# Kernel optimization log

Hardware: AMD Instinct MI355X
Metric: run time of the kernel (lower is better)

The kernel has to match this reference:

```python
import jax, jax.numpy as jnp
import numpy as np

N_NODES = 100000
N_EDGES = 1600000
K_IND = 16          # num_indicator_weight (distance bins)
K_MLP = 16          # num_mlp_weight
DIM_HIDDEN = 64     # dim_mlp_hidden
DIST_MAX = 1.0      # distance_max
K = K_IND + K_MLP   # node feature dim / Dense output dim


def setup_inputs() -> dict:
    key = jax.random.key(0)
    ks = jax.random.split(key, 10)
    nodes = jax.random.normal(ks[0], (N_NODES, K), dtype=jnp.float32)
    distance = jax.random.uniform(ks[1], (N_EDGES,), dtype=jnp.float32) * DIST_MAX
    receivers = jnp.sort(jax.random.randint(ks[2], (N_EDGES,), 0, N_NODES, dtype=jnp.int32))
    senders = jax.random.randint(ks[3], (N_EDGES,), 0, N_NODES, dtype=jnp.int32)
    edges_padding = jnp.ones((N_EDGES,), dtype=jnp.float32)
    # MLPWeights params (Dense(1->H), Dense(H->K_MLP))
    w1 = jax.random.normal(ks[4], (1, DIM_HIDDEN), dtype=jnp.float32) / np.sqrt(1.0)
    b1 = jnp.zeros((DIM_HIDDEN,), dtype=jnp.float32)
    w2 = jax.random.normal(ks[5], (DIM_HIDDEN, K_MLP), dtype=jnp.float32) / np.sqrt(DIM_HIDDEN)
    b2 = jnp.zeros((K_MLP,), dtype=jnp.float32)
    # PowerDifference params (a=0.5, b=2)
    a = jnp.array([0.5], dtype=jnp.float32)
    b = jnp.array([2.0], dtype=jnp.float32)
    # gamma_self (no bias), gamma_gathered (with bias), both Dense(K->K)
    wg_self = jax.random.normal(ks[6], (K, K), dtype=jnp.float32) / np.sqrt(K)
    wg_gath = jax.random.normal(ks[7], (K, K), dtype=jnp.float32) / np.sqrt(K)
    bg_gath = jnp.zeros((K,), dtype=jnp.float32)
    return {"nodes": nodes, "distance": distance, "edges_padding": edges_padding,
            "receivers": receivers, "senders": senders,
            "w1": w1, "b1": b1, "w2": w2, "b2": b2,
            "a": a, "b": b, "wg_self": wg_self, "wg_gath": wg_gath, "bg_gath": bg_gath}


def _normalize_edges(edges, seg_ids, num_segments):
    sums = jax.ops.segment_sum(edges, seg_ids, num_segments=num_segments, indices_are_sorted=True)
    return edges / (sums[seg_ids] + 1e-5)


def _softmax_edges(edges, seg_ids, num_segments):
    maxs = jax.ops.segment_max(edges, seg_ids, num_segments=num_segments, indices_are_sorted=True)
    e = jnp.exp(edges - maxs[seg_ids])
    sums = jax.ops.segment_sum(e, seg_ids, num_segments=num_segments, indices_are_sorted=True)
    return e / sums[seg_ids]


def reference(nodes, distance, edges_padding, receivers, senders,
              w1, b1, w2, b2, a, b, wg_self, wg_gath, bg_gath):
    n = nodes.shape[0]
    d = distance[:, None]                                   # [E,1]
    # IndicatorWeights: bin membership via heaviside of product
    bins = jnp.linspace(0.0, DIST_MAX, K_IND + 1, dtype=nodes.dtype)
    indicator = jnp.heaviside((bins[None, :-1] - d) * (d - bins[None, 1:]), 0.0)  # [E,K_IND]
    indicator_w = _normalize_edges(indicator, receivers, n)
    # MLPWeights: Dense -> relu -> Dense, then segment softmax
    mlp = jax.nn.relu(d @ w1 + b1) @ w2 + b2                # [E,K_MLP]
    mlp_w = _softmax_edges(mlp, receivers, n)
    weights = jnp.concatenate([indicator_w, mlp_w], axis=1) * edges_padding[:, None]  # [E,K]
    # PowerDifference on gathered node pairs
    a_c = jnp.clip(a, 0.0, 1.0)
    b_c = jnp.abs(b)
    edge_pds = jnp.power(jnp.abs(a_c * nodes[receivers] - (1.0 - a_c) * nodes[senders]), b_c)  # [E,K]
    gathered = jax.ops.segment_sum(weights * edge_pds, receivers, num_segments=n, indices_are_sorted=True)  # [N,K]
    out = jax.nn.relu(nodes @ wg_self + (gathered @ wg_gath + bg_gath))
    return out
```

## Files before the change

kernel.cpp:

```cpp
#include <hip/hip_runtime.h>
#include <math.h>

#define K_TOT 32
#define K_IND 16
#define K_MLP 16
#define DHID  64
#define M_NODES 4
#define LOG2E 1.44269504088896340736f

template<bool B> struct BoolC { static constexpr bool value = B; };

__device__ __forceinline__ float fast_rcp(float x) {
    float r; asm("v_rcp_f32 %0, %1" : "=v"(r) : "v"(x)); return r;
}
__device__ __forceinline__ float fast_exp2(float x) {
    float r; asm("v_exp_f32 %0, %1" : "=v"(r) : "v"(x)); return r;
}


__global__ void prep_kernel(const int* __restrict__ recv, int E, int N,
                            const float* __restrict__ w1,
                            const float* __restrict__ b1,
                            const float* __restrict__ w2,
                            const float* __restrict__ padv,
                            float* __restrict__ wsP,
                            float* __restrict__ wsN,
                            int* __restrict__ wsflag,
                            int* __restrict__ viol,
                            int* __restrict__ rp) {
    if (blockIdx.x == 0 && threadIdx.x < 64) {
        int t = threadIdx.x;
        if (t < K_MLP) {
            float P = 0.f, Nn = 0.f;
            for (int j = 0; j < DHID; ++j) {
                float w = w1[j];
                float v = w2[j * K_MLP + t];
                P  += fmaxf(w, 0.f) * v;
                Nn += fminf(w, 0.f) * v;
            }
            wsP[t] = P; wsN[t] = Nn;
        }
        bool nz = (b1[t] != 0.f);
        unsigned long long mask = __ballot(nz);
        if (t == 0) *wsflag = (mask == 0ull) ? 1 : 0;
    }
    int e = blockIdx.x * blockDim.x + threadIdx.x;
    bool ok = (e < E) ? (padv[e] == 1.0f) : true;
    if (!__all((int)ok)) {
        if ((threadIdx.x & 63) == 0) atomicOr(viol, 1);
    }
    if (e < E) {
        int r0 = recv[e];
        int r1 = (e + 1 < E) ? recv[e + 1] : N;
        if (e == 0) {
            for (int t = 0; t <= r0; ++t) rp[t] = 0;
        }
        for (int t = r0 + 1; t <= r1; ++t) rp[t] = e + 1;
    }
}

__global__ __launch_bounds__(256) void graph_kernel(
        const float* __restrict__ nodes,
        const float* __restrict__ dist,
        const float* __restrict__ padv,
        const int*   __restrict__ send,
        const float* __restrict__ w1,
        const float* __restrict__ b1,
        const float* __restrict__ w2,
        const float* __restrict__ b2,
        const float* __restrict__ a_p,
        const float* __restrict__ b_p,
        const float* __restrict__ wg_self,
        const float* __restrict__ wg_gath,
        const float* __restrict__ bg,
        const float* __restrict__ wsP,
        const float* __restrict__ wsN,
        const int*   __restrict__ wsflag,
        const int*   __restrict__ viol,
        const int*   __restrict__ rp,
        float* __restrict__ out,
        int N, int E) {
    __shared__ __align__(16) float2 s_wp[1024];
    __shared__ __align__(16) float2 s_gn[4][32][4];

    {
        int t = threadIdx.x;
        float4 ws4 = ((const float4*)wg_self)[t];
        float4 wg4 = ((const float4*)wg_gath)[t];
        s_wp[t * 4 + 0] = make_float2(ws4.x, wg4.x);
        s_wp[t * 4 + 1] = make_float2(ws4.y, wg4.y);
        s_wp[t * 4 + 2] = make_float2(ws4.z, wg4.z);
        s_wp[t * 4 + 3] = make_float2(ws4.w, wg4.w);
    }
    __syncthreads();

    int wv   = threadIdx.x >> 6;
    int wave = blockIdx.x * 4 + wv;
    int n0   = wave * M_NODES;
    if (n0 >= N) return;

    int lane = threadIdx.x & 63;
    int eg   = lane >> 4;
    int cc   = lane & 15;

    float a_c = fminf(fmaxf(a_p[0], 0.f), 1.f);
    float am  = 1.f - a_c;
    float bc  = fabsf(b_p[0]);

    float Pk = wsP[cc];
    float Nk = wsN[cc];
    float Pk2 = Pk * LOG2E;
    float Nk2 = Nk * LOG2E;
    float negM2 = -fmaxf(fabsf(Pk2), fabsf(Nk2));

    float lo = (float)cc * 0.0625f;
    float hi = lo + 0.0625f;

    int fastflag = (*wsflag != 0) && (bc == 2.0f);
    int allpad   = (*viol == 0);
    float bgv = bg[lane & 31];

    int rl = rp[min(n0 + min(lane, 4), N)];
    int e0k[5];
#pragma unroll
    for (int k = 0; k < 5; ++k) e0k[k] = __shfl(rl, k);
    int lenk[4]; int maxlen = 0;
#pragma unroll
    for (int k = 0; k < 4; ++k) {
        lenk[k] = e0k[k + 1] - e0k[k];
        maxlen = max(maxlen, lenk[k]);
    }

    int cap = N * K_TOT - 1;
    float rowA = nodes[min(n0 * K_TOT + lane, cap)];
    float rowB = nodes[min(n0 * K_TOT + 64 + lane, cap)];

    auto fast4 = [&](auto APC) {
        constexpr bool ALLPAD = decltype(APC)::value;
        float dC, peC = 1.f; int sC;
        {
            int li = min(lane, max(lenk[0] - 1, 0));
            int ei = min(e0k[0] + li, E - 1);
            dC = dist[ei]; sC = send[ei];
            if (!ALLPAD) peC = padv[ei];
        }
#pragma unroll
        for (int k = 0; k < 4; ++k) {
            float dNx = 0.f, peNx = 1.f; int sNx = 0;
            if (k < 3) {
                int li = min(lane, max(lenk[k + 1] - 1, 0));
                int ei = min(e0k[k + 1] + li, E - 1);
                dNx = dist[ei]; sNx = send[ei];
                if (!ALLPAD) peNx = padv[ei];
            }
            int len = lenk[k];
            float d_all  = (lane < len) ? dC : 2.0f;
            int   s_all  = sC;
            float pe_all = peC;
            (void)pe_all;

            float nsrc = (k < 2) ? rowA : rowB;
            float nr0 = __shfl(nsrc, (k & 1) * 32 + cc);
            float nr1 = __shfl(nsrc, (k & 1) * 32 + cc + 16);
            float anr0 = a_c * nr0;
            float anr1 = a_c * nr1;

            float cnt = 0.f, si = 0.f, l = 0.f, acc = 0.f;
            if (len > 0) {
                int nG = (len + 3) >> 2;

#define GRP_BODY(G)                                                          \
                {                                                            \
                    int i = ((G) << 2) + eg;                                 \
                    bool valid = i < len;                                    \
                    float d  = __shfl(d_all, i);                             \
                    int   s  = __shfl(s_all, i);                             \
                    float pe = ALLPAD ? 1.0f : __shfl(pe_all, i);            \
                    const float* nsrow = nodes + (s * K_TOT + cc);           \
                    float ns0 = nsrow[0];                                    \
                    float ns1 = nsrow[16];                                   \
                    float t0 = fmaf(-am, ns0, anr0);                         \
                    float t1 = fmaf(-am, ns1, anr1);                         \
                    float pd0 = t0 * t0;                                     \
                    float pd1 = t1 * t1;                                     \
                    bool inb = (d > lo) && (d < hi);                         \
                    if (ALLPAD) {                                            \
                        float mb = inb ? 1.f : 0.f;                          \
                        cnt += mb;                                           \
                        si   = fmaf(mb, pd0, si);                            \
                    } else {                                                 \
                        cnt += inb ? 1.f : 0.f;                              \
                        si   = inb ? fmaf(pe, pd0, si) : si;                 \
                    }                                                        \
                    float q2 = (d > 0.f) ? Pk2 : Nk2;                        \
                    float p = fast_exp2(fmaf(d, q2, negM2));                 \
                    p = valid ? p : 0.f;                                     \
                    l += p;                                                  \
                    acc = ALLPAD ? fmaf(p, pd1, acc)                         \
                                 : fmaf(p, pe * pd1, acc);                   \
                }

                int g = 0;
                for (; g + 2 <= nG; g += 2) {
                    GRP_BODY(g)
                    GRP_BODY(g + 1)
                }
                if (g < nG) {
                    GRP_BODY(g)
                }
#undef GRP_BODY
            }

#pragma unroll
            for (int off = 16; off <= 32; off <<= 1) {
                cnt += __shfl_xor(cnt, off);
                si  += __shfl_xor(si,  off);
                l   += __shfl_xor(l,   off);
                acc += __shfl_xor(acc, off);
            }
            float g_ind = si * fast_rcp(cnt + 1e-5f);
            float g_mlp = (l > 0.f) ? (acc * fast_rcp(l)) : 0.f;

            float pre_g = ((lane >> 4) & 1) ? g_mlp : g_ind;
            float pre_n = ((lane >> 4) & 1) ? nr1 : nr0;
            if (lane < 32) s_gn[wv][lane][k] = make_float2(pre_n, pre_g);

            dC = dNx; sC = sNx; peC = peNx;
        }
    };

    if (__builtin_amdgcn_readfirstlane((int)(fastflag && (maxlen <= 64)))) {
        if (__builtin_amdgcn_readfirstlane(allpad)) fast4(BoolC<true>{});
        else                                        fast4(BoolC<false>{});
    } else {
        for (int k = 0; k < 4; ++k) {
            int len = lenk[k], e0 = e0k[k];
            float nsrc = (k < 2) ? rowA : rowB;
            float nr0 = __shfl(nsrc, (k & 1) * 32 + cc);
            float nr1 = __shfl(nsrc, (k & 1) * 32 + cc + 16);
            float anr0 = a_c * nr0;
            float anr1 = a_c * nr1;

            float cnt = 0.f, si = 0.f, l = 0.f, acc = 0.f;
            float m_on = -INFINITY;
            for (int i = eg; i < len; i += 4) {
                int e = e0 + i;
                float d  = dist[e];
                int   s  = send[e];
                float pe = padv[e];
                const float* nsrow = nodes + (s * K_TOT + cc);
                float ns0 = nsrow[0];
                float ns1 = nsrow[16];
                float t0 = fabsf(fmaf(-am, ns0, anr0));
                float t1 = fabsf(fmaf(-am, ns1, anr1));
                float pd0 = powf(t0, bc);
                float pd1 = powf(t1, bc);

                bool inb = (d > lo) && (d < hi);
                cnt += inb ? 1.f : 0.f;
                si  += inb ? pe * pd0 : 0.f;

                float mlp = 0.f;
                for (int j = 0; j < DHID; ++j) {
                    float h2 = fmaxf(fmaf(d, w1[j], b1[j]), 0.f);
                    mlp = fmaf(h2, w2[j * K_MLP + cc], mlp);
                }
                float mn = fmaxf(m_on, mlp);
                float al = (m_on == -INFINITY) ? 0.f : __expf(m_on - mn);
                float p  = __expf(mlp - mn);
                l   = fmaf(l, al, p);
                acc = fmaf(acc, al, p * pe * pd1);
                m_on = mn;
            }
#pragma unroll
            for (int off = 16; off <= 32; off <<= 1) {
                cnt += __shfl_xor(cnt, off);
                si  += __shfl_xor(si,  off);
                float m2 = __shfl_xor(m_on, off), l2 = __shfl_xor(l, off), a2 = __shfl_xor(acc, off);
                float mn = fmaxf(m_on, m2);
                float f1 = (m_on == -INFINITY) ? 0.f : __expf(m_on - mn);
                float f2 = (m2   == -INFINITY) ? 0.f : __expf(m2 - mn);
                l   = l * f1 + l2 * f2;
                acc = acc * f1 + a2 * f2;
                m_on = mn;
            }
            float g_ind = si / (cnt + 1e-5f);
            float g_mlp = (l > 0.f) ? (acc / l) : 0.f;

            float pre_g = ((lane >> 4) & 1) ? g_mlp : g_ind;
            float pre_n = ((lane >> 4) & 1) ? nr1 : nr0;
            if (lane < 32) s_gn[wv][lane][k] = make_float2(pre_n, pre_g);
        }
    }

    int h  = lane >> 5;
    int oc = lane & 31;
    const float2* wpp = &s_wp[(h * 16) * K_TOT + oc];
    const float2 (* __restrict__ sgw)[4] = s_gn[wv];

    float o0 = 0.f, o1 = 0.f, o2 = 0.f, o3 = 0.f;
#pragma unroll
    for (int jj = 0; jj < 16; ++jj) {
        float2 w   = wpp[jj * K_TOT];
        float4 v01 = *reinterpret_cast<const float4*>(&sgw[h * 16 + jj][0]);
        float4 v23 = *reinterpret_cast<const float4*>(&sgw[h * 16 + jj][2]);
        o0 = fmaf(v01.x, w.x, o0); o0 = fmaf(v01.y, w.y, o0);
        o1 = fmaf(v01.z, w.x, o1); o1 = fmaf(v01.w, w.y, o1);
        o2 = fmaf(v23.x, w.x, o2); o2 = fmaf(v23.y, w.y, o2);
        o3 = fmaf(v23.z, w.x, o3); o3 = fmaf(v23.w, w.y, o3);
    }
    o0 += __shfl_xor(o0, 32);
    o1 += __shfl_xor(o1, 32);
    o2 += __shfl_xor(o2, 32);
    o3 += __shfl_xor(o3, 32);
    o0 = fmaxf(o0 + bgv, 0.f);
    o1 = fmaxf(o1 + bgv, 0.f);
    o2 = fmaxf(o2 + bgv, 0.f);
    o3 = fmaxf(o3 + bgv, 0.f);

    float st0 = (lane >= 32) ? o1 : o0;
    float st1 = (lane >= 32) ? o3 : o2;
    int   b5  = lane >> 5;
    if (n0 + b5 < N)     out[n0 * K_TOT + lane]      = st0;
    if (n0 + 2 + b5 < N) out[n0 * K_TOT + 64 + lane] = st1;
}

extern "C" void kernel_launch(void* const* d_in, const int* in_sizes, int n_in,
                              void* d_out, int out_size, void* d_ws, size_t ws_size,
                              hipStream_t stream) {
    const float* nodes   = (const float*)d_in[0];
    const float* dist    = (const float*)d_in[1];
    const float* padv    = (const float*)d_in[2];
    const int*   recv    = (const int*)d_in[3];
    const int*   send    = (const int*)d_in[4];
    const float* w1      = (const float*)d_in[5];
    const float* b1      = (const float*)d_in[6];
    const float* w2      = (const float*)d_in[7];
    const float* b2      = (const float*)d_in[8];
    const float* a_p     = (const float*)d_in[9];
    const float* b_p     = (const float*)d_in[10];
    const float* wg_self = (const float*)d_in[11];
    const float* wg_gath = (const float*)d_in[12];
    const float* bg      = (const float*)d_in[13];
    float* out = (float*)d_out;

    int N = in_sizes[0] / K_TOT;
    int E = in_sizes[1];

    float* wsf    = (float*)d_ws;
    float* wsP    = wsf;
    float* wsN    = wsf + 16;
    int*   wsflag = (int*)d_ws + 32;
    int*   viol   = (int*)d_ws + 33;
    int*   rp     = (int*)d_ws + 64;

    hipMemsetAsync(viol, 0, sizeof(int), stream);

    prep_kernel<<<(E + 255) / 256, 256, 0, stream>>>(recv, E, N, w1, b1, w2,
                                                     padv, wsP, wsN, wsflag,
                                                     viol, rp);
    int waves = (N + M_NODES - 1) / M_NODES;
    graph_kernel<<<(waves + 3) / 4, 256, 0, stream>>>(
        nodes, dist, padv, send, w1, b1, w2, b2, a_p, b_p,
        wg_self, wg_gath, bg, wsP, wsN, wsflag, viol, rp, out, N, E);
}
```

Baseline: 144.5 us.

## Load edge data directly per group and specialize softmax for nonnegative distances

The fast path no longer stages distance and sender values in registers and broadcasts them with shuffles. Each edge group now loads dist/send straight from memory at a wave-uniform base, and a touch-prefetch warms the next node's edges. The prep kernel also checks that all distances are nonnegative, which lets the simple path drop the sign select and use a tighter softmax shift. The maxlen<=64 limit goes away, and node rows are loaded with scalar-uniform addresses instead of shuffles. This trades shuffle traffic for more direct global loads and adds one extra pass over dist in prep.

```diff
diff --git a/kernel.cpp b/kernel.cpp
--- a/kernel.cpp
+++ b/kernel.cpp
@@ -23,6 +23,7 @@
                             const float* __restrict__ b1,
                             const float* __restrict__ w2,
                             const float* __restrict__ padv,
+                            const float* __restrict__ dist,
                             float* __restrict__ wsP,
                             float* __restrict__ wsN,
                             int* __restrict__ wsflag,
@@ -45,9 +46,13 @@
         if (t == 0) *wsflag = (mask == 0ull) ? 1 : 0;
     }
     int e = blockIdx.x * blockDim.x + threadIdx.x;
-    bool ok = (e < E) ? (padv[e] == 1.0f) : true;
-    if (!__all((int)ok)) {
+    bool okp = (e < E) ? (padv[e] == 1.0f) : true;
+    if (!__all((int)okp)) {
         if ((threadIdx.x & 63) == 0) atomicOr(viol, 1);
+    }
+    bool okd = (e < E) ? (dist[e] >= 0.0f) : true;
+    if (!__all((int)okd)) {
+        if ((threadIdx.x & 63) == 0) atomicOr(viol, 2);
     }
     if (e < E) {
         int r0 = recv[e];
@@ -111,104 +116,128 @@
     float Nk = wsN[cc];
     float Pk2 = Pk * LOG2E;
     float Nk2 = Nk * LOG2E;
-    float negM2 = -fmaxf(fabsf(Pk2), fabsf(Nk2));
+    float negMs = -fabsf(Pk2);
+    float negMg = fminf(negMs, -fabsf(Nk2));
 
     float lo = (float)cc * 0.0625f;
     float hi = lo + 0.0625f;
 
     int fastflag = (*wsflag != 0) && (bc == 2.0f);
-    int allpad   = (*viol == 0);
+    int simple   = fastflag && (*viol == 0);
     float bgv = bg[lane & 31];
 
     int rl = rp[min(n0 + min(lane, 4), N)];
     int e0k[5];
 #pragma unroll
     for (int k = 0; k < 5; ++k) e0k[k] = __shfl(rl, k);
-    int lenk[4]; int maxlen = 0;
-#pragma unroll
-    for (int k = 0; k < 4; ++k) {
-        lenk[k] = e0k[k + 1] - e0k[k];
-        maxlen = max(maxlen, lenk[k]);
-    }
-
-    int cap = N * K_TOT - 1;
-    float rowA = nodes[min(n0 * K_TOT + lane, cap)];
-    float rowB = nodes[min(n0 * K_TOT + 64 + lane, cap)];
-
-    auto fast4 = [&](auto APC) {
-        constexpr bool ALLPAD = decltype(APC)::value;
-        float dC, peC = 1.f; int sC;
-        {
-            int li = min(lane, max(lenk[0] - 1, 0));
-            int ei = min(e0k[0] + li, E - 1);
-            dC = dist[ei]; sC = send[ei];
-            if (!ALLPAD) peC = padv[ei];
-        }
+    int lenk[4];
+#pragma unroll
+    for (int k = 0; k < 4; ++k) lenk[k] = e0k[k + 1] - e0k[k];
+
+    auto fast4 = [&](auto SC) {
+        constexpr bool SIMPLE = decltype(SC)::value;
+        int nu0 = __builtin_amdgcn_readfirstlane(min(n0, N - 1));
+        float nr0C = nodes[nu0 * K_TOT + cc];
+        float nr1C = nodes[nu0 * K_TOT + cc + 16];
 #pragma unroll
         for (int k = 0; k < 4; ++k) {
-            float dNx = 0.f, peNx = 1.f; int sNx = 0;
+            float nr0N = 0.f, nr1N = 0.f;
             if (k < 3) {
-                int li = min(lane, max(lenk[k + 1] - 1, 0));
-                int ei = min(e0k[k + 1] + li, E - 1);
-                dNx = dist[ei]; sNx = send[ei];
-                if (!ALLPAD) peNx = padv[ei];
+                int nu1 = __builtin_amdgcn_readfirstlane(min(n0 + k + 1, N - 1));
+                nr0N = nodes[nu1 * K_TOT + cc];
+                nr1N = nodes[nu1 * K_TOT + cc + 16];
+                int pfi = min(e0k[k + 1] + (lane & 48), E - 1);
+                float dpf = dist[pfi];
+                int   spf = send[pfi];
+                asm volatile("" :: "v"(dpf), "v"(spf));
             }
             int len = lenk[k];
-            float d_all  = (lane < len) ? dC : 2.0f;
-            int   s_all  = sC;
-            float pe_all = peC;
-            (void)pe_all;
-
-            float nsrc = (k < 2) ? rowA : rowB;
-            float nr0 = __shfl(nsrc, (k & 1) * 32 + cc);
-            float nr1 = __shfl(nsrc, (k & 1) * 32 + cc + 16);
-            float anr0 = a_c * nr0;
-            float anr1 = a_c * nr1;
+            int e0u = __builtin_amdgcn_readfirstlane(e0k[k]);
+            const float* db = dist + e0u;
+            const int*   sb = send + e0u;
+            const float* pb = padv + e0u;
+            (void)pb;
+
+            float anr0 = a_c * nr0C;
+            float anr1 = a_c * nr1C;
 
             float cnt = 0.f, si = 0.f, l = 0.f, acc = 0.f;
-            if (len > 0) {
-                int nG = (len + 3) >> 2;
-
-#define GRP_BODY(G)                                                          \
-                {                                                            \
-                    int i = ((G) << 2) + eg;                                 \
-                    bool valid = i < len;                                    \
-                    float d  = __shfl(d_all, i);                             \
-                    int   s  = __shfl(s_all, i);                             \
-                    float pe = ALLPAD ? 1.0f : __shfl(pe_all, i);            \
-                    const float* nsrow = nodes + (s * K_TOT + cc);           \
-                    float ns0 = nsrow[0];                                    \
-                    float ns1 = nsrow[16];                                   \
-                    float t0 = fmaf(-am, ns0, anr0);                         \
-                    float t1 = fmaf(-am, ns1, anr1);                         \
-                    float pd0 = t0 * t0;                                     \
-                    float pd1 = t1 * t1;                                     \
-                    bool inb = (d > lo) && (d < hi);                         \
-                    if (ALLPAD) {                                            \
-                        float mb = inb ? 1.f : 0.f;                          \
-                        cnt += mb;                                           \
-                        si   = fmaf(mb, pd0, si);                            \
-                    } else {                                                 \
-                        cnt += inb ? 1.f : 0.f;                              \
-                        si   = inb ? fmaf(pe, pd0, si) : si;                 \
-                    }                                                        \
+
+#define FB(G)                                                                \
+            {                                                                \
+                int idx = ((G) << 2) + eg;                                   \
+                float d  = db[idx];                                          \
+                int   s  = sb[idx];                                          \
+                float pe = SIMPLE ? 1.0f : pb[idx];                          \
+                const float* nsrow = nodes + (s * K_TOT + cc);               \
+                float ns0 = nsrow[0];                                        \
+                float ns1 = nsrow[16];                                       \
+                float t0 = fmaf(-am, ns0, anr0);                             \
+                float t1 = fmaf(-am, ns1, anr1);                             \
+                float pd0 = t0 * t0;                                         \
+                float pd1 = t1 * t1;                                         \
+                bool inb = (d > lo) && (d < hi);                             \
+                if (SIMPLE) {                                                \
+                    float mb = inb ? 1.f : 0.f;                              \
+                    cnt += mb;                                               \
+                    si   = fmaf(mb, pd0, si);                                \
+                    float p = fast_exp2(fmaf(d, Pk2, negMs));                \
+                    l += p;                                                  \
+                    acc = fmaf(p, pd1, acc);                                 \
+                } else {                                                     \
+                    cnt += inb ? 1.f : 0.f;                                  \
+                    si   = inb ? fmaf(pe, pd0, si) : si;                     \
                     float q2 = (d > 0.f) ? Pk2 : Nk2;                        \
-                    float p = fast_exp2(fmaf(d, q2, negM2));                 \
-                    p = valid ? p : 0.f;                                     \
+                    float p = fast_exp2(fmaf(d, q2, negMg));                 \
                     l += p;                                                  \
-                    acc = ALLPAD ? fmaf(p, pd1, acc)                         \
-                                 : fmaf(p, pe * pd1, acc);                   \
+                    acc = fmaf(p, pe * pd1, acc);                            \
+                }                                                            \
+            }
+
+            int nGf = len >> 2;
+            int rem = len & 3;
+            int g = 0;
+            for (; g + 2 <= nGf; g += 2) {
+                FB(g)
+                FB(g + 1)
+            }
+            if (g < nGf) {
+                FB(g)
+            }
+#undef FB
+            if (rem) {
+                int i  = (nGf << 2) + eg;
+                int ii = min(i, len - 1);
+                float d  = db[ii];
+                int   s  = sb[ii];
+                float pe = SIMPLE ? 1.0f : pb[ii];
+                const float* nsrow = nodes + (s * K_TOT + cc);
+                float ns0 = nsrow[0];
+                float ns1 = nsrow[16];
+                float t0 = fmaf(-am, ns0, anr0);
+                float t1 = fmaf(-am, ns1, anr1);
+                float pd0 = t0 * t0;
+                float pd1 = t1 * t1;
+                bool valid = i < len;
+                bool inb = valid && (d > lo) && (d < hi);
+                float p;
+                if (SIMPLE) {
+                    float mb = inb ? 1.f : 0.f;
+                    cnt += mb;
+                    si   = fmaf(mb, pd0, si);
+                    p = fast_exp2(fmaf(d, Pk2, negMs));
+                    p = valid ? p : 0.f;
+                    l += p;
+                    acc = fmaf(p, pd1, acc);
+                } else {
+                    cnt += inb ? 1.f : 0.f;
+                    si   = inb ? fmaf(pe, pd0, si) : si;
+                    float q2 = (d > 0.f) ? Pk2 : Nk2;
+                    p = fast_exp2(fmaf(d, q2, negMg));
+                    p = valid ? p : 0.f;
+                    l += p;
+                    acc = fmaf(p, pe * pd1, acc);
                 }
-
-                int g = 0;
-                for (; g + 2 <= nG; g += 2) {
-                    GRP_BODY(g)
-                    GRP_BODY(g + 1)
-                }
-                if (g < nG) {
-                    GRP_BODY(g)
-                }
-#undef GRP_BODY
             }
 
 #pragma unroll
@@ -222,22 +251,22 @@
             float g_mlp = (l > 0.f) ? (acc * fast_rcp(l)) : 0.f;
 
             float pre_g = ((lane >> 4) & 1) ? g_mlp : g_ind;
-            float pre_n = ((lane >> 4) & 1) ? nr1 : nr0;
+            float pre_n = ((lane >> 4) & 1) ? nr1C : nr0C;
             if (lane < 32) s_gn[wv][lane][k] = make_float2(pre_n, pre_g);
 
-            dC = dNx; sC = sNx; peC = peNx;
+            nr0C = nr0N; nr1C = nr1N;
         }
     };
 
-    if (__builtin_amdgcn_readfirstlane((int)(fastflag && (maxlen <= 64)))) {
-        if (__builtin_amdgcn_readfirstlane(allpad)) fast4(BoolC<true>{});
+    if (__builtin_amdgcn_readfirstlane(fastflag)) {
+        if (__builtin_amdgcn_readfirstlane(simple)) fast4(BoolC<true>{});
         else                                        fast4(BoolC<false>{});
     } else {
         for (int k = 0; k < 4; ++k) {
             int len = lenk[k], e0 = e0k[k];
-            float nsrc = (k < 2) ? rowA : rowB;
-            float nr0 = __shfl(nsrc, (k & 1) * 32 + cc);
-            float nr1 = __shfl(nsrc, (k & 1) * 32 + cc + 16);
+            int nu = __builtin_amdgcn_readfirstlane(min(n0 + k, N - 1));
+            float nr0 = nodes[nu * K_TOT + cc];
+            float nr1 = nodes[nu * K_TOT + cc + 16];
             float anr0 = a_c * nr0;
             float anr1 = a_c * nr1;
 
@@ -357,8 +386,8 @@
     hipMemsetAsync(viol, 0, sizeof(int), stream);
 
     prep_kernel<<<(E + 255) / 256, 256, 0, stream>>>(recv, E, N, w1, b1, w2,
-                                                     padv, wsP, wsN, wsflag,
-                                                     viol, rp);
+                                                     padv, dist, wsP, wsN,
+                                                     wsflag, viol, rp);
     int waves = (N + M_NODES - 1) / M_NODES;
     graph_kernel<<<(waves + 3) / 4, 256, 0, stream>>>(
         nodes, dist, padv, send, w1, b1, w2, b2, a_p, b_p,
```

After: 156.2 us. 1.08x slower.
